# Kernel optimization log

Hardware: AMD Instinct MI355X
Metric: run time of the kernel (lower is better)

Reference implementation:

```python
import jax, jax.numpy as jnp
import numpy as np

H = 16          # num_attention_heads
D = 64          # attention_head_size
ATT_SPAN = 256  # position_buckets (pos_ebd_size)
MAX_POS = 512   # max_relative_positions
LN_EPS = 1e-7


def _build_rel_pos(q_len, k_len, bucket_size=ATT_SPAN, max_position=MAX_POS):
    """Log-bucketed relative positions, shape [q_len, k_len], int32."""
    rel = np.arange(q_len)[:, None] - np.arange(k_len)[None, :]
    sign = np.sign(rel)
    mid = bucket_size // 2
    abs_pos = np.where((rel < mid) & (rel > -mid), mid - 1, np.abs(rel)).astype(np.float64)
    log_pos = np.ceil(np.log(abs_pos / mid) / np.log((max_position - 1) / mid) * (mid - 1)) + mid
    bucket_pos = np.where(abs_pos <= mid, rel.astype(np.float64), log_pos * sign)
    return jnp.asarray(bucket_pos.astype(np.int32))


def setup_inputs() -> dict:
    key = jax.random.key(0)
    ks = jax.random.split(key, 12)
    B, N, HID = 4, 1024, H * D
    s = 0.02
    inp = {
        "hidden_states": jax.random.normal(ks[0], (B, N, HID), jnp.float32),
        "attention_mask": jnp.ones((B, N, N), dtype=bool),
        "rel_embeddings": jax.random.normal(ks[1], (2 * ATT_SPAN, HID), jnp.float32),
        "Wq": jax.random.normal(ks[2], (HID, HID), jnp.float32) * s,
        "bq": jnp.zeros((HID,), jnp.float32),
        "Wk": jax.random.normal(ks[3], (HID, HID), jnp.float32) * s,
        "bk": jnp.zeros((HID,), jnp.float32),
        "Wv": jax.random.normal(ks[4], (HID, HID), jnp.float32) * s,
        "bv": jnp.zeros((HID,), jnp.float32),
        "Wo": jax.random.normal(ks[5], (HID, HID), jnp.float32) * s,
        "bo": jnp.zeros((HID,), jnp.float32),
        "ln_gamma": jnp.ones((HID,), jnp.float32),
        "ln_beta": jnp.zeros((HID,), jnp.float32),
    }
    return inp


def _heads(x):
    # [B, N, H*D] -> [B, H, N, D]
    B, N, _ = x.shape
    return x.reshape(B, N, H, D).transpose(0, 2, 1, 3)


def _forward(hidden_states, attention_mask, rel_embeddings,
             Wq, bq, Wk, bk, Wv, bv, Wo, bo, ln_gamma, ln_beta):
    B, N, HID = hidden_states.shape
    scale_factor = 3  # 1 + c2p + p2c
    scale = jnp.sqrt(jnp.float32(D * scale_factor))

    q = _heads(hidden_states @ Wq.T + bq)  # [B,H,N,D]
    k = _heads(hidden_states @ Wk.T + bk)
    v = _heads(hidden_states @ Wv.T + bv)

    scores = jnp.einsum("bhqd,bhkd->bhqk", q, k / scale)  # [B,H,N,N]

    # --- disentangled attention bias ---
    rel_pos = _build_rel_pos(N, N)                       # [N,N] int32
    rel_emb = rel_embeddings[: 2 * ATT_SPAN]             # [2S, HID]
    # share_att_key=True: reuse query/key projections for positions
    pos_k = (rel_emb @ Wk.T + bk).reshape(2 * ATT_SPAN, H, D).transpose(1, 0, 2)  # [H,2S,D]
    pos_q = (rel_emb @ Wq.T + bq).reshape(2 * ATT_SPAN, H, D).transpose(1, 0, 2)  # [H,2S,D]

    # c2p: query x pos_key, gather along position axis
    c2p = jnp.einsum("bhqd,hsd->bhqs", q, pos_k)          # [B,H,N,2S]
    c2p_idx = jnp.clip(rel_pos + ATT_SPAN, 0, 2 * ATT_SPAN - 1)  # [N,N]
    c2p = jnp.take_along_axis(c2p, jnp.broadcast_to(c2p_idx[None, None], (B, H, N, N)), axis=-1)
    scores = scores + c2p / scale

    # p2c: key x pos_query, gather then transpose
    p2c = jnp.einsum("bhkd,hsd->bhks", k, pos_q)          # [B,H,N,2S]
    p2c_idx = jnp.clip(-rel_pos + ATT_SPAN, 0, 2 * ATT_SPAN - 1)
    p2c = jnp.take_along_axis(p2c, jnp.broadcast_to(p2c_idx[None, None], (B, H, N, N)), axis=-1)
    scores = scores + jnp.swapaxes(p2c, -1, -2) / scale

    # --- XSoftmax: masked softmax ---
    mask = attention_mask[:, None, :, :]                  # [B,1,N,N] bool
    neg = jnp.finfo(scores.dtype).min
    probs = jax.nn.softmax(jnp.where(mask, scores, neg), axis=-1)
    probs = jnp.where(mask, probs, 0.0)

    ctx = jnp.einsum("bhqk,bhkd->bhqd", probs, v)         # [B,H,N,D]
    ctx = ctx.transpose(0, 2, 1, 3).reshape(B, N, HID)

    # --- DebertaV2SelfOutput: dense + residual + LayerNorm ---
    out = ctx @ Wo.T + bo + hidden_states
    mu = out.mean(-1, keepdims=True)
    var = ((out - mu) ** 2).mean(-1, keepdims=True)
    out = (out - mu) * jax.lax.rsqrt(var + LN_EPS) * ln_gamma + ln_beta
    return out


def reference(hidden_states, attention_mask, rel_embeddings,
              Wq, bq, Wk, bk, Wv, bv, Wo, bo, ln_gamma, ln_beta):
    return _forward(hidden_states, attention_mask, rel_embeddings,
                    Wq, bq, Wk, bk, Wv, bv, Wo, bo, ln_gamma, ln_beta)
```

## Files before the change

kernel.cpp:

```cpp
#include <hip/hip_runtime.h>
#include <cstdint>
#include <cstddef>


#define Bn   4
#define Nn   1024
#define Hh   16
#define Dd   64
#define HIDn 1024
#define S2n  512
#define QSZ  4194304

typedef unsigned short u16;
typedef __attribute__((ext_vector_type(8))) short short8;
typedef __attribute__((ext_vector_type(4))) float floatx4;

__device__ __forceinline__ float b2f(u16 u) {
    union { unsigned int i; float f; } v; v.i = ((unsigned int)u) << 16; return v.f;
}
__device__ __forceinline__ u16 f2b(float f) {
    union { float f; unsigned int i; } v; v.f = f;
    unsigned int r = v.i + 0x7fffu + ((v.i >> 16) & 1u);
    return (u16)(r >> 16);
}

__global__ void rel_table_kernel(int* __restrict__ relIdx) {
    for (int d = threadIdx.x; d < 2047; d += blockDim.x) {
        int delta = d - 1023;
        int sg = (delta > 0) - (delta < 0);
        int ad = delta < 0 ? -delta : delta;
        double abs_pos = (delta < 128 && delta > -128) ? 127.0 : (double)ad;
        double log_pos = ceil(log(abs_pos / 128.0) / log(511.0 / 128.0) * 127.0) + 128.0;
        double bucket = (abs_pos <= 128.0) ? (double)delta : log_pos * (double)sg;
        int idx = (int)bucket + 256;
        idx = idx < 0 ? 0 : (idx > 511 ? 511 : idx);
        relIdx[d] = idx;
    }
}

__global__ __launch_bounds__(256)
void pack_kernel(const float* __restrict__ X, const float* __restrict__ relEmb,
                 const float* __restrict__ Wq, const float* __restrict__ Wk,
                 const float* __restrict__ Wv, const float* __restrict__ Wo,
                 const float* __restrict__ bq, const float* __restrict__ bk,
                 const float* __restrict__ bv,
                 u16* __restrict__ Xb, u16* __restrict__ relEmbB,
                 u16* __restrict__ Wqkv, u16* __restrict__ WoB,
                 float* __restrict__ bqkv)
{
    const int i = blockIdx.x * 256 + threadIdx.x;
    const int NX = 4194304, NW = 1048576, NR = 524288;
    if (i < NX) Xb[i] = f2b(X[i]);
    if (i < NW) {
        Wqkv[i]          = f2b(Wq[i]);
        Wqkv[NW + i]     = f2b(Wk[i]);
        Wqkv[2 * NW + i] = f2b(Wv[i]);
        WoB[i]           = f2b(Wo[i]);
    }
    if (i < NR) relEmbB[i] = f2b(relEmb[i]);
    if (i < 1024) { bqkv[i] = bq[i]; bqkv[1024 + i] = bk[i]; bqkv[2048 + i] = bv[i]; }
}

template<int MODE>
__global__ __launch_bounds__(256)
void gemm_bt(const u16* __restrict__ A, const u16* __restrict__ Bm,
             const float* __restrict__ bias, const float* __restrict__ resid,
             void* __restrict__ outv, int K)
{
    __shared__ __align__(16) u16 SH[2 * 128 * 72];
    u16* As = SH;
    u16* Bs = SH + 128 * 72;
    const int tid = threadIdx.x;
    const int w = tid >> 6, lane = tid & 63, quad = lane >> 4, r = lane & 15;
    const int wm = (w >> 1) * 64, wn = (w & 1) * 64;
    const int m0 = blockIdx.y * 128, n0 = blockIdx.x * 128;
    const int srow = tid >> 1, scs = (tid & 1) * 32;

    floatx4 acc[4][4];
    #pragma unroll
    for (int i = 0; i < 4; i++)
        #pragma unroll
        for (int j = 0; j < 4; j++)
            acc[i][j] = (floatx4){0.f, 0.f, 0.f, 0.f};

    for (int k0 = 0; k0 < K; k0 += 64) {
        const u16* ap = A  + (size_t)(m0 + srow) * K + k0 + scs;
        const u16* bp = Bm + (size_t)(n0 + srow) * K + k0 + scs;
        uint4 a0 = *(const uint4*)ap,        a1 = *(const uint4*)(ap + 8);
        uint4 a2 = *(const uint4*)(ap + 16), a3 = *(const uint4*)(ap + 24);
        uint4 b0 = *(const uint4*)bp,        b1 = *(const uint4*)(bp + 8);
        uint4 b2 = *(const uint4*)(bp + 16), b3 = *(const uint4*)(bp + 24);
        *(uint4*)&As[srow * 72 + scs]      = a0;
        *(uint4*)&As[srow * 72 + scs + 8]  = a1;
        *(uint4*)&As[srow * 72 + scs + 16] = a2;
        *(uint4*)&As[srow * 72 + scs + 24] = a3;
        *(uint4*)&Bs[srow * 72 + scs]      = b0;
        *(uint4*)&Bs[srow * 72 + scs + 8]  = b1;
        *(uint4*)&Bs[srow * 72 + scs + 16] = b2;
        *(uint4*)&Bs[srow * 72 + scs + 24] = b3;
        __syncthreads();
        #pragma unroll
        for (int ks = 0; ks < 2; ks++) {
            short8 af[4], bf[4];
            #pragma unroll
            for (int mi = 0; mi < 4; mi++)
                af[mi] = *(const short8*)&As[(wm + mi * 16 + r) * 72 + ks * 32 + quad * 8];
            #pragma unroll
            for (int ni = 0; ni < 4; ni++)
                bf[ni] = *(const short8*)&Bs[(wn + ni * 16 + r) * 72 + ks * 32 + quad * 8];
            #pragma unroll
            for (int mi = 0; mi < 4; mi++)
                #pragma unroll
                for (int ni = 0; ni < 4; ni++)
                    acc[mi][ni] = __builtin_amdgcn_mfma_f32_16x16x32_bf16(
                        af[mi], bf[ni], acc[mi][ni], 0, 0, 0);
        }
        __syncthreads();
    }

    if (MODE == 0 && n0 >= 2048) {
        u16* CT = SH;
        #pragma unroll
        for (int mi = 0; mi < 4; mi++)
            #pragma unroll
            for (int ni = 0; ni < 4; ni++) {
                int n_loc = wn + ni * 16 + r;
                float bv = bias[n0 + n_loc];
                #pragma unroll
                for (int reg = 0; reg < 4; reg++) {
                    int m_loc = wm + mi * 16 + quad * 4 + reg;
                    CT[n_loc * 136 + m_loc] = f2b(acc[mi][ni][reg] + bv);
                }
            }
        __syncthreads();
        const int nr = tid >> 1, half = tid & 1;
        const int nn = (n0 - 2048) + nr;
        const int hh = nn >> 6, dd = nn & 63, bb = m0 >> 10;
        const int tok0 = (m0 & 1023) + half * 64;
        u16* dst = (u16*)outv + (size_t)2 * QSZ +
                   (((size_t)(bb * Hh + hh)) * Dd + dd) * Nn + tok0;
        const u16* srcl = &CT[nr * 136 + half * 64];
        #pragma unroll
        for (int j = 0; j < 8; j++)
            *(uint4*)(dst + j * 8) = *(const uint4*)(srcl + j * 8);
        return;
    }

    #pragma unroll
    for (int mi = 0; mi < 4; mi++) {
        #pragma unroll
        for (int ni = 0; ni < 4; ni++) {
            int n = n0 + wn + ni * 16 + r;
            float bv = bias[n];
            #pragma unroll
            for (int reg = 0; reg < 4; reg++) {
                int m = m0 + wm + mi * 16 + quad * 4 + reg;
                float val = acc[mi][ni][reg] + bv;
                if (MODE == 0) {
                    int which = n >> 10, nn = n & 1023;
                    int hh = nn >> 6, dd = nn & 63, bb = m >> 10, tok = m & 1023;
                    ((u16*)outv)[(size_t)which * QSZ +
                                 (((size_t)(bb * Hh + hh)) * Nn + tok) * Dd + dd] = f2b(val);
                } else if (MODE == 1) {
                    int hh = n >> 6, dd = n & 63;
                    ((u16*)outv)[((size_t)hh * S2n + m) * Dd + dd] = f2b(val);
                } else {
                    ((float*)outv)[(size_t)m * HIDn + n] =
                        val + resid[(size_t)m * HIDn + n];
                }
            }
        }
    }
}

__global__ __launch_bounds__(256, 3)
void attn_fused(const u16* __restrict__ Qh, const u16* __restrict__ Kh,
                const u16* __restrict__ Vt, const u16* __restrict__ posK,
                const u16* __restrict__ posQ, const int* __restrict__ relIdx,
                u16* __restrict__ ctxB)
{
    __shared__ __align__(16) u16 U1[64][72];
    __shared__ __align__(16) u16 U2[64][72];
    __shared__            u16 c2pW[64][132];
    __shared__            u16 p2cW[64][132];
    __shared__ int   relW[128];

    const int q0 = blockIdx.x * 64, h = blockIdx.y, b = blockIdx.z;
    const int hb = b * Hh + h;
    const int tid = threadIdx.x;
    const int w = tid >> 6, lane = tid & 63, quad = lane >> 4, r = lane & 15;
    const int row = tid >> 2, co = (tid & 3) * 16;

    const u16* Qp = Qh + (size_t)hb * Nn * Dd;
    const u16* Kp = Kh + (size_t)hb * Nn * Dd;
    const u16* Vp = Vt + (size_t)hb * Dd * Nn;
    const u16* pK = posK + (size_t)h * S2n * Dd;
    const u16* pQ = posQ + (size_t)h * S2n * Dd;

    short8 qf0[4], qf1[4];
    #pragma unroll
    for (int mi = 0; mi < 4; mi++) {
        const u16* src = Qp + (size_t)(q0 + mi * 16 + r) * Dd + quad * 8;
        qf0[mi] = *(const short8*)src;
        qf1[mi] = *(const short8*)(src + 32);
    }
    short8 aq0, aq1;
    {
        const u16* src = Qp + (size_t)(q0 + (w << 4) + r) * Dd + quad * 8;
        aq0 = *(const short8*)src;
        aq1 = *(const short8*)(src + 32);
    }

    floatx4 Oacc[4];
    #pragma unroll
    for (int ni = 0; ni < 4; ni++) Oacc[ni] = (floatx4){0.f, 0.f, 0.f, 0.f};
    floatx4 lacc = (floatx4){0.f, 0.f, 0.f, 0.f};
    short8 ones;
    #pragma unroll
    for (int j = 0; j < 8; j++) ones[j] = (short)0x3F80;

    const float inv_scale = 0.07216878364870323f;
    const int k_l = (w << 4) + r;

    short8 kb0, kb1;
    uint4 vC0, vC1;
    {
        const u16* ksrc = Kp + (size_t)k_l * Dd + quad * 8;
        kb0 = *(const short8*)ksrc; kb1 = *(const short8*)(ksrc + 32);
        const u16* vsrc = Vp + (size_t)row * Nn + co;
        vC0 = *(const uint4*)vsrc; vC1 = *(const uint4*)(vsrc + 8);
    }

    for (int kt = 0; kt < 16; kt++) {
        const int k0 = kt * 64;
        const int base = q0 - k0 + 960;
        const int i0 = relIdx[base];
        const int i1 = relIdx[base + 126];
        const int chunks = ((i1 - i0 + 1) + 15) >> 4;
        const int rows1 = chunks < 4 ? chunks * 16 : 64;

        {
            if (tid < 127) relW[tid] = relIdx[base + tid];
            if (row < rows1) {
                const u16* pk = pK + (size_t)(i0 + row) * Dd + co;
                const u16* pq = pQ + (size_t)(i0 + row) * Dd + co;
                *(uint4*)&U1[row][co]     = *(const uint4*)pk;
                *(uint4*)&U1[row][co + 8] = *(const uint4*)(pk + 8);
                *(uint4*)&U2[row][co]     = *(const uint4*)pq;
                *(uint4*)&U2[row][co + 8] = *(const uint4*)(pq + 8);
            }
        }
        __syncthreads();

        short8 kN0, kN1;
        uint4 vN0, vN1;
        {
            const int kn = (kt < 15) ? (k0 + 64) : k0;
            const u16* ksrc = Kp + (size_t)(kn + k_l) * Dd + quad * 8;
            kN0 = *(const short8*)ksrc; kN1 = *(const short8*)(ksrc + 32);
            const u16* vsrc = Vp + (size_t)row * Nn + kn + co;
            vN0 = *(const uint4*)vsrc; vN1 = *(const uint4*)(vsrc + 8);
        }

        floatx4 S[4];
        #pragma unroll
        for (int mi = 0; mi < 4; mi++) S[mi] = (floatx4){0.f, 0.f, 0.f, 0.f};
        #pragma unroll
        for (int mi = 0; mi < 4; mi++) {
            S[mi] = __builtin_amdgcn_mfma_f32_16x16x32_bf16(qf0[mi], kb0, S[mi], 0, 0, 0);
            S[mi] = __builtin_amdgcn_mfma_f32_16x16x32_bf16(qf1[mi], kb1, S[mi], 0, 0, 0);
        }
        {
            const int ch1 = chunks < 4 ? chunks : 4;
            for (int ci = 0; ci < ch1; ci++) {
                short8 pk0 = *(const short8*)&U1[ci * 16 + r][quad * 8];
                short8 pk1 = *(const short8*)&U1[ci * 16 + r][32 + quad * 8];
                short8 pq0 = *(const short8*)&U2[ci * 16 + r][quad * 8];
                short8 pq1 = *(const short8*)&U2[ci * 16 + r][32 + quad * 8];
                floatx4 dc = (floatx4){0.f, 0.f, 0.f, 0.f};
                floatx4 dp = (floatx4){0.f, 0.f, 0.f, 0.f};
                dc = __builtin_amdgcn_mfma_f32_16x16x32_bf16(aq0, pk0, dc, 0, 0, 0);
                dc = __builtin_amdgcn_mfma_f32_16x16x32_bf16(aq1, pk1, dc, 0, 0, 0);
                dp = __builtin_amdgcn_mfma_f32_16x16x32_bf16(kb0, pq0, dp, 0, 0, 0);
                dp = __builtin_amdgcn_mfma_f32_16x16x32_bf16(kb1, pq1, dp, 0, 0, 0);
                #pragma unroll
                for (int reg = 0; reg < 4; reg++) {
                    c2pW[(w << 4) + (quad << 2) + reg][ci * 16 + r] = f2b(dc[reg]);
                    p2cW[(w << 4) + (quad << 2) + reg][ci * 16 + r] = f2b(dp[reg]);
                }
            }
        }
        if (chunks > 4) {
            __syncthreads();
            const int rows2 = chunks * 16 - 64;
            if (row < rows2) {
                const u16* pk = pK + (size_t)(i0 + 64 + row) * Dd + co;
                const u16* pq = pQ + (size_t)(i0 + 64 + row) * Dd + co;
                *(uint4*)&U1[row][co]     = *(const uint4*)pk;
                *(uint4*)&U1[row][co + 8] = *(const uint4*)(pk + 8);
                *(uint4*)&U2[row][co]     = *(const uint4*)pq;
                *(uint4*)&U2[row][co + 8] = *(const uint4*)(pq + 8);
            }
            __syncthreads();
            for (int ci = 4; ci < chunks; ci++) {
                short8 pk0 = *(const short8*)&U1[(ci - 4) * 16 + r][quad * 8];
                short8 pk1 = *(const short8*)&U1[(ci - 4) * 16 + r][32 + quad * 8];
                short8 pq0 = *(const short8*)&U2[(ci - 4) * 16 + r][quad * 8];
                short8 pq1 = *(const short8*)&U2[(ci - 4) * 16 + r][32 + quad * 8];
                floatx4 dc = (floatx4){0.f, 0.f, 0.f, 0.f};
                floatx4 dp = (floatx4){0.f, 0.f, 0.f, 0.f};
                dc = __builtin_amdgcn_mfma_f32_16x16x32_bf16(aq0, pk0, dc, 0, 0, 0);
                dc = __builtin_amdgcn_mfma_f32_16x16x32_bf16(aq1, pk1, dc, 0, 0, 0);
                dp = __builtin_amdgcn_mfma_f32_16x16x32_bf16(kb0, pq0, dp, 0, 0, 0);
                dp = __builtin_amdgcn_mfma_f32_16x16x32_bf16(kb1, pq1, dp, 0, 0, 0);
                #pragma unroll
                for (int reg = 0; reg < 4; reg++) {
                    c2pW[(w << 4) + (quad << 2) + reg][ci * 16 + r] = f2b(dc[reg]);
                    p2cW[(w << 4) + (quad << 2) + reg][ci * 16 + r] = f2b(dp[reg]);
                }
            }
        }
        __syncthreads();

        {
            *(uint4*)&U2[row][co]     = vC0;
            *(uint4*)&U2[row][co + 8] = vC1;
        }
        #pragma unroll
        for (int mi = 0; mi < 4; mi++) {
            #pragma unroll
            for (int reg = 0; reg < 4; reg++) {
                int q_l = mi * 16 + (quad << 2) + reg;
                int j = relW[q_l - k_l + 63] - i0;
                float cv = b2f(c2pW[q_l][j]);
                float pv = b2f(p2cW[k_l][j]);
                float p = __expf((S[mi][reg] + cv + pv) * inv_scale);
                U1[q_l][k_l] = f2b(p);
            }
        }
        __syncthreads();

        {
            short8 pa0 = *(const short8*)&U1[k_l][quad * 8];
            short8 pa1 = *(const short8*)&U1[k_l][32 + quad * 8];
            #pragma unroll
            for (int ni = 0; ni < 4; ni++) {
                short8 vb0 = *(const short8*)&U2[ni * 16 + r][quad * 8];
                short8 vb1 = *(const short8*)&U2[ni * 16 + r][32 + quad * 8];
                Oacc[ni] = __builtin_amdgcn_mfma_f32_16x16x32_bf16(pa0, vb0, Oacc[ni], 0, 0, 0);
                Oacc[ni] = __builtin_amdgcn_mfma_f32_16x16x32_bf16(pa1, vb1, Oacc[ni], 0, 0, 0);
            }
            lacc = __builtin_amdgcn_mfma_f32_16x16x32_bf16(pa0, ones, lacc, 0, 0, 0);
            lacc = __builtin_amdgcn_mfma_f32_16x16x32_bf16(pa1, ones, lacc, 0, 0, 0);
        }
        __syncthreads();

        kb0 = kN0; kb1 = kN1; vC0 = vN0; vC1 = vN1;
    }

    float invl[4];
    #pragma unroll
    for (int reg = 0; reg < 4; reg++) invl[reg] = 1.0f / lacc[reg];
    #pragma unroll
    for (int ni = 0; ni < 4; ni++) {
        int d = ni * 16 + r;
        #pragma unroll
        for (int reg = 0; reg < 4; reg++) {
            int q = (w << 4) + (quad << 2) + reg;
            ctxB[((size_t)(b * Nn + q0 + q)) * HIDn + h * Dd + d] =
                f2b(Oacc[ni][reg] * invl[reg]);
        }
    }
}

__global__ __launch_bounds__(256)
void ln_kernel(const float* __restrict__ xin, const float* __restrict__ gamma,
               const float* __restrict__ beta, float* __restrict__ outp)
{
    const int rowi = blockIdx.x;
    const int tid = threadIdx.x;
    const float* x = xin + (size_t)rowi * HIDn;
    float4 v = *(const float4*)(x + tid * 4);
    float s  = v.x + v.y + v.z + v.w;
    float ss = v.x*v.x + v.y*v.y + v.z*v.z + v.w*v.w;
    #pragma unroll
    for (int off = 32; off > 0; off >>= 1) {
        s  += __shfl_down(s, off);
        ss += __shfl_down(ss, off);
    }
    __shared__ float red[4], red2[4], mb[2];
    const int wv = tid >> 6;
    if ((tid & 63) == 0) { red[wv] = s; red2[wv] = ss; }
    __syncthreads();
    if (tid == 0) {
        float a = red[0] + red[1] + red[2] + red[3];
        float q = red2[0] + red2[1] + red2[2] + red2[3];
        float mean = a * (1.0f / 1024.0f);
        float var = q * (1.0f / 1024.0f) - mean * mean;
        mb[0] = mean;
        mb[1] = rsqrtf(var + 1e-7f);
    }
    __syncthreads();
    float mean = mb[0], rstd = mb[1];
    float xv[4] = {v.x, v.y, v.z, v.w};
    float* o = outp + (size_t)rowi * HIDn + tid * 4;
    #pragma unroll
    for (int j = 0; j < 4; j++)
        o[j] = (xv[j] - mean) * rstd * gamma[tid * 4 + j] + beta[tid * 4 + j];
}

extern "C" void kernel_launch(void* const* d_in, const int* in_sizes, int n_in,
                              void* d_out, int out_size, void* d_ws, size_t ws_size,
                              hipStream_t stream)
{
    const float* X      = (const float*)d_in[0];
    const float* relEmb = (const float*)d_in[2];
    const float* Wq = (const float*)d_in[3];  const float* bq = (const float*)d_in[4];
    const float* Wk = (const float*)d_in[5];  const float* bk = (const float*)d_in[6];
    const float* Wv = (const float*)d_in[7];  const float* bv = (const float*)d_in[8];
    const float* Wo = (const float*)d_in[9];  const float* bo = (const float*)d_in[10];
    const float* gamma = (const float*)d_in[11];
    const float* beta  = (const float*)d_in[12];
    float* outp = (float*)d_out;
    (void)in_sizes; (void)n_in; (void)out_size; (void)ws_size;

    char* ws = (char*)d_ws;
    size_t off = 0;
    auto alloc = [&](size_t bytes) -> char* {
        char* p = ws + off;
        off = (off + bytes + 255) & ~(size_t)255;
        return p;
    };
    int*   relIdx  = (int*)alloc(2047 * sizeof(int));
    u16*   Xb      = (u16*)alloc((size_t)4194304 * 2);
    u16*   Wqkv    = (u16*)alloc((size_t)3 * 1048576 * 2);
    u16*   WoB     = (u16*)alloc((size_t)1048576 * 2);
    u16*   relEmbB = (u16*)alloc((size_t)524288 * 2);
    float* bqkv    = (float*)alloc(3072 * 4);
    u16*   QKV     = (u16*)alloc((size_t)3 * QSZ * 2);
    u16*   posK    = (u16*)alloc(((size_t)Hh * S2n + 16) * Dd * 2);
    u16*   posQ    = (u16*)alloc(((size_t)Hh * S2n + 16) * Dd * 2);
    u16*   ctxB    = (u16*)alloc((size_t)4194304 * 2);
    float* out_pre = (float*)alloc((size_t)4194304 * 4);

    dim3 blk(256);
    hipLaunchKernelGGL(rel_table_kernel, dim3(1), blk, 0, stream, relIdx);
    pack_kernel<<<dim3(16384), blk, 0, stream>>>(X, relEmb, Wq, Wk, Wv, Wo,
                                                 bq, bk, bv, Xb, relEmbB, Wqkv,
                                                 WoB, bqkv);

    gemm_bt<0><<<dim3(24, 32), blk, 0, stream>>>(Xb, Wqkv, bqkv, nullptr, QKV, HIDn);
    gemm_bt<1><<<dim3(8, 4), blk, 0, stream>>>(relEmbB, Wqkv + 1048576, bqkv + 1024,
                                               nullptr, posK, HIDn);
    gemm_bt<1><<<dim3(8, 4), blk, 0, stream>>>(relEmbB, Wqkv, bqkv,
                                               nullptr, posQ, HIDn);

    attn_fused<<<dim3(16, 16, 4), blk, 0, stream>>>(QKV, QKV + QSZ, QKV + 2 * QSZ,
                                                    posK, posQ, relIdx, ctxB);

    gemm_bt<2><<<dim3(8, 32), blk, 0, stream>>>(ctxB, WoB, bo, X, out_pre, HIDn);
    ln_kernel<<<dim3(4096), blk, 0, stream>>>(out_pre, gamma, beta, outp);
}
```

Measured before the change: 336.9 us.

## Prefetch GEMM tiles into registers, use lighter barriers, merge pos projection GEMMs

The GEMM main loop now issues the next k-tile's global loads into registers before the MFMA work on the current tile, so global-memory latency overlaps compute. Every __syncthreads in the GEMM and attention kernels becomes a barrier that waits only on LDS counters (lgkmcnt), leaving outstanding global loads in flight across the barrier. The two position-projection GEMMs are merged into one launch (MODE 3) that writes posQ and posK by column range, saving a launch. The cost is higher register pressure from the prefetch buffers, and the custom barrier relies on nothing needing a vmcnt wait at those points.

```diff
diff --git a/kernel.cpp b/kernel.cpp
--- a/kernel.cpp
+++ b/kernel.cpp
@@ -22,6 +22,12 @@
     union { float f; unsigned int i; } v; v.f = f;
     unsigned int r = v.i + 0x7fffu + ((v.i >> 16) & 1u);
     return (u16)(r >> 16);
+}
+
+__device__ __forceinline__ void bar_lds() {
+    asm volatile("s_waitcnt lgkmcnt(0)" ::: "memory");
+    __builtin_amdgcn_s_barrier();
+    asm volatile("" ::: "memory");
 }
 
 __global__ void rel_table_kernel(int* __restrict__ relIdx) {
@@ -83,13 +89,17 @@
         for (int j = 0; j < 4; j++)
             acc[i][j] = (floatx4){0.f, 0.f, 0.f, 0.f};
 
+    uint4 a0, a1, a2, a3, b0, b1, b2, b3;
+    {
+        const u16* ap = A  + (size_t)(m0 + srow) * K + scs;
+        const u16* bp = Bm + (size_t)(n0 + srow) * K + scs;
+        a0 = *(const uint4*)ap;        a1 = *(const uint4*)(ap + 8);
+        a2 = *(const uint4*)(ap + 16); a3 = *(const uint4*)(ap + 24);
+        b0 = *(const uint4*)bp;        b1 = *(const uint4*)(bp + 8);
+        b2 = *(const uint4*)(bp + 16); b3 = *(const uint4*)(bp + 24);
+    }
+
     for (int k0 = 0; k0 < K; k0 += 64) {
-        const u16* ap = A  + (size_t)(m0 + srow) * K + k0 + scs;
-        const u16* bp = Bm + (size_t)(n0 + srow) * K + k0 + scs;
-        uint4 a0 = *(const uint4*)ap,        a1 = *(const uint4*)(ap + 8);
-        uint4 a2 = *(const uint4*)(ap + 16), a3 = *(const uint4*)(ap + 24);
-        uint4 b0 = *(const uint4*)bp,        b1 = *(const uint4*)(bp + 8);
-        uint4 b2 = *(const uint4*)(bp + 16), b3 = *(const uint4*)(bp + 24);
         *(uint4*)&As[srow * 72 + scs]      = a0;
         *(uint4*)&As[srow * 72 + scs + 8]  = a1;
         *(uint4*)&As[srow * 72 + scs + 16] = a2;
@@ -98,7 +108,19 @@
         *(uint4*)&Bs[srow * 72 + scs + 8]  = b1;
         *(uint4*)&Bs[srow * 72 + scs + 16] = b2;
         *(uint4*)&Bs[srow * 72 + scs + 24] = b3;
-        __syncthreads();
+        bar_lds();
+
+        uint4 na0 = a0, na1 = a1, na2 = a2, na3 = a3;
+        uint4 nb0 = b0, nb1 = b1, nb2 = b2, nb3 = b3;
+        if (k0 + 64 < K) {
+            const u16* ap = A  + (size_t)(m0 + srow) * K + k0 + 64 + scs;
+            const u16* bp = Bm + (size_t)(n0 + srow) * K + k0 + 64 + scs;
+            na0 = *(const uint4*)ap;        na1 = *(const uint4*)(ap + 8);
+            na2 = *(const uint4*)(ap + 16); na3 = *(const uint4*)(ap + 24);
+            nb0 = *(const uint4*)bp;        nb1 = *(const uint4*)(bp + 8);
+            nb2 = *(const uint4*)(bp + 16); nb3 = *(const uint4*)(bp + 24);
+        }
+
         #pragma unroll
         for (int ks = 0; ks < 2; ks++) {
             short8 af[4], bf[4];
@@ -115,7 +137,9 @@
                     acc[mi][ni] = __builtin_amdgcn_mfma_f32_16x16x32_bf16(
                         af[mi], bf[ni], acc[mi][ni], 0, 0, 0);
         }
-        __syncthreads();
+        bar_lds();
+        a0 = na0; a1 = na1; a2 = na2; a3 = na3;
+        b0 = nb0; b1 = nb1; b2 = nb2; b3 = nb3;
     }
 
     if (MODE == 0 && n0 >= 2048) {
@@ -132,7 +156,7 @@
                     CT[n_loc * 136 + m_loc] = f2b(acc[mi][ni][reg] + bv);
                 }
             }
-        __syncthreads();
+        bar_lds();
         const int nr = tid >> 1, half = tid & 1;
         const int nn = (n0 - 2048) + nr;
         const int hh = nn >> 6, dd = nn & 63, bb = m0 >> 10;
@@ -164,6 +188,12 @@
                 } else if (MODE == 1) {
                     int hh = n >> 6, dd = n & 63;
                     ((u16*)outv)[((size_t)hh * S2n + m) * Dd + dd] = f2b(val);
+                } else if (MODE == 3) {
+                    int which = n >> 10, nn = n & 1023;
+                    int hh = nn >> 6, dd = nn & 63;
+                    u16* dst = which ? (u16*)(void*)(const_cast<float*>(resid))
+                                     : (u16*)outv;
+                    dst[((size_t)hh * S2n + m) * Dd + dd] = f2b(val);
                 } else {
                     ((float*)outv)[(size_t)m * HIDn + n] =
                         val + resid[(size_t)m * HIDn + n];
@@ -250,7 +280,7 @@
                 *(uint4*)&U2[row][co + 8] = *(const uint4*)(pq + 8);
             }
         }
-        __syncthreads();
+        bar_lds();
 
         short8 kN0, kN1;
         uint4 vN0, vN1;
@@ -291,7 +321,7 @@
             }
         }
         if (chunks > 4) {
-            __syncthreads();
+            bar_lds();
             const int rows2 = chunks * 16 - 64;
             if (row < rows2) {
                 const u16* pk = pK + (size_t)(i0 + 64 + row) * Dd + co;
@@ -301,7 +331,7 @@
                 *(uint4*)&U2[row][co]     = *(const uint4*)pq;
                 *(uint4*)&U2[row][co + 8] = *(const uint4*)(pq + 8);
             }
-            __syncthreads();
+            bar_lds();
             for (int ci = 4; ci < chunks; ci++) {
                 short8 pk0 = *(const short8*)&U1[(ci - 4) * 16 + r][quad * 8];
                 short8 pk1 = *(const short8*)&U1[(ci - 4) * 16 + r][32 + quad * 8];
@@ -320,7 +350,7 @@
                 }
             }
         }
-        __syncthreads();
+        bar_lds();
 
         {
             *(uint4*)&U2[row][co]     = vC0;
@@ -338,7 +368,7 @@
                 U1[q_l][k_l] = f2b(p);
             }
         }
-        __syncthreads();
+        bar_lds();
 
         {
             short8 pa0 = *(const short8*)&U1[k_l][quad * 8];
@@ -353,7 +383,7 @@
             lacc = __builtin_amdgcn_mfma_f32_16x16x32_bf16(pa0, ones, lacc, 0, 0, 0);
             lacc = __builtin_amdgcn_mfma_f32_16x16x32_bf16(pa1, ones, lacc, 0, 0, 0);
         }
-        __syncthreads();
+        bar_lds();
 
         kb0 = kN0; kb1 = kN1; vC0 = vN0; vC1 = vN1;
     }
@@ -450,10 +480,8 @@
                                                  WoB, bqkv);
 
     gemm_bt<0><<<dim3(24, 32), blk, 0, stream>>>(Xb, Wqkv, bqkv, nullptr, QKV, HIDn);
-    gemm_bt<1><<<dim3(8, 4), blk, 0, stream>>>(relEmbB, Wqkv + 1048576, bqkv + 1024,
-                                               nullptr, posK, HIDn);
-    gemm_bt<1><<<dim3(8, 4), blk, 0, stream>>>(relEmbB, Wqkv, bqkv,
-                                               nullptr, posQ, HIDn);
+    gemm_bt<3><<<dim3(16, 4), blk, 0, stream>>>(relEmbB, Wqkv, bqkv,
+                                                (const float*)posK, posQ, HIDn);
 
     attn_fused<<<dim3(16, 16, 4), blk, 0, stream>>>(QKV, QKV + QSZ, QKV + 2 * QSZ,
                                                     posK, posQ, relIdx, ctxB);
```

Result: faster. 305.6 us (-9.3%).
